# Kernel optimization log

Measured on AMD Instinct MI355X. Metric: run time of the kernel, lower is better.

Reference implementation:

```python
import jax, jax.numpy as jnp
import numpy as np

EMBED_DIM = 1024
NUM_HEADS = 16
HEAD_DIM = EMBED_DIM // NUM_HEADS  # 64


def setup_inputs() -> dict:
    key = jax.random.key(0)
    ks = jax.random.split(key, 9)
    B, S, D, Hd = 2, 2048, EMBED_DIM, HEAD_DIM
    s_in = 1.0 / np.sqrt(D)
    s_out = 1.0 / np.sqrt(D)
    return {
        "x": jax.random.normal(ks[0], (B, S, D), dtype=jnp.float32),
        # weights stored [in, out] (transpose of torch Linear.weight)
        "wq": jax.random.uniform(ks[1], (D, D), jnp.float32, -s_in, s_in),
        "bq": jax.random.uniform(ks[2], (D,), jnp.float32, -s_in, s_in),
        "wk": jax.random.uniform(ks[3], (D, Hd), jnp.float32, -s_in, s_in),
        "bk": jax.random.uniform(ks[4], (Hd,), jnp.float32, -s_in, s_in),
        "wv": jax.random.uniform(ks[5], (D, Hd), jnp.float32, -s_in, s_in),
        "bv": jax.random.uniform(ks[6], (Hd,), jnp.float32, -s_in, s_in),
        "wo": jax.random.uniform(ks[7], (D, D), jnp.float32, -s_out, s_out),
        "bo": jax.random.uniform(ks[8], (D,), jnp.float32, -s_out, s_out),
    }


def reference(x, wq, bq, wk, bk, wv, bv, wo, bo):
    B, S, D = x.shape
    H, Hd = NUM_HEADS, HEAD_DIM
    q = (x @ wq + bq).reshape(B, S, H, Hd)  # per-head queries
    k = x @ wk + bk                          # shared single-head keys  [B,S,Hd]
    v = x @ wv + bv                          # shared single-head values [B,S,Hd]
    # NOTE: original scales by embed_dim**-0.5 (not head_dim) — keep faithful.
    scores = jnp.einsum('bqhd,bkd->bhqk', q, k) / jnp.sqrt(jnp.float32(D))
    attn = jax.nn.softmax(scores, axis=-1)
    out = jnp.einsum('bhqk,bkd->bqhd', attn, v).reshape(B, S, D)
    return out @ wo + bo
```

## Files before the change

### kernel.cpp

```cpp
#include <hip/hip_runtime.h>

typedef unsigned short ushort_t;
typedef __attribute__((ext_vector_type(8))) short short8;
typedef __attribute__((ext_vector_type(4))) float f32x4;

#define EMBED 1024
#define NHEADS 16
#define HDIM 64
#define SEQ 2048
#define BATCH 2
#define BS (BATCH*SEQ)
#define QSCALE 0.045084234f

static __device__ __forceinline__ ushort_t f2b(float x) {
    union { float f; unsigned u; } v; v.f = x;
    unsigned r = v.u + 0x7FFFu + ((v.u >> 16) & 1u);
    return (ushort_t)(r >> 16);
}

static __device__ __forceinline__ void gload_lds16(const void* g, void* l) {
    __builtin_amdgcn_global_load_lds(
        (const __attribute__((address_space(1))) void*)g,
        (__attribute__((address_space(3))) void*)l, 16, 0, 0);
}

static __device__ __forceinline__ float exp2_raw(float x) {
    float r;
    asm("v_exp_f32 %0, %1" : "=v"(r) : "v"(x));
    return r;
}

__global__ __launch_bounds__(256) void prep_kernel(
    const float* __restrict__ x,
    const float* __restrict__ wq, const float* __restrict__ wk,
    const float* __restrict__ wv, const float* __restrict__ wo,
    ushort_t* __restrict__ xb, ushort_t* __restrict__ wqkv_t,
    ushort_t* __restrict__ wo_t)
{
    __shared__ float LsT[64][65];
    const int bid = blockIdx.x;
    const int t = threadIdx.x;

    if (bid < 2048) {
        const size_t i = ((size_t)bid * 256 + t) * 8;
        float4 f0 = *reinterpret_cast<const float4*>(x + i);
        float4 f1 = *reinterpret_cast<const float4*>(x + i + 4);
        short8 h;
        h[0] = (short)f2b(f0.x); h[1] = (short)f2b(f0.y);
        h[2] = (short)f2b(f0.z); h[3] = (short)f2b(f0.w);
        h[4] = (short)f2b(f1.x); h[5] = (short)f2b(f1.y);
        h[6] = (short)f2b(f1.z); h[7] = (short)f2b(f1.w);
        *reinterpret_cast<short8*>(xb + i) = h;
        return;
    }

    const float* src; ushort_t* dst; int N, bx, by;
    if (bid < 2304)      { int r = bid - 2048; src = wq; dst = wqkv_t;            N = 1024; bx = r & 15; by = r >> 4; }
    else if (bid < 2320) { int r = bid - 2304; src = wk; dst = wqkv_t + 1024*1024; N = 64;  bx = 0;      by = r; }
    else if (bid < 2336) { int r = bid - 2320; src = wv; dst = wqkv_t + 1088*1024; N = 64;  bx = 0;      by = r; }
    else                 { int r = bid - 2336; src = wo; dst = wo_t;              N = 1024; bx = r & 15; by = r >> 4; }
    const int n0 = bx * 64, k0 = by * 64;
    const int rr0 = t >> 4;
    const int c4 = (t & 15) * 4;
    #pragma unroll
    for (int rr = 0; rr < 4; ++rr) {
        float4 f = *reinterpret_cast<const float4*>(
            src + (size_t)(k0 + rr0 + rr * 16) * N + n0 + c4);
        LsT[c4 + 0][rr0 + rr * 16] = f.x;
        LsT[c4 + 1][rr0 + rr * 16] = f.y;
        LsT[c4 + 2][rr0 + rr * 16] = f.z;
        LsT[c4 + 3][rr0 + rr * 16] = f.w;
    }
    __syncthreads();
    const int rn = t >> 2;
    const int c16 = (t & 3) * 16;
    ushort_t* d = dst + (size_t)(n0 + rn) * 1024 + k0 + c16;
    short8 h0, h1;
    #pragma unroll
    for (int i = 0; i < 8; ++i) h0[i] = (short)f2b(LsT[rn][c16 + i]);
    #pragma unroll
    for (int i = 0; i < 8; ++i) h1[i] = (short)f2b(LsT[rn][c16 + 8 + i]);
    *reinterpret_cast<short8*>(d) = h0;
    *reinterpret_cast<short8*>(d + 8) = h1;
}

template<int MODE>
__global__ __launch_bounds__(256, 3) void mfma_gemm(
    const ushort_t* __restrict__ A, const ushort_t* __restrict__ Bt,
    const float* __restrict__ b0, const float* __restrict__ b1,
    const float* __restrict__ b2,
    float* __restrict__ Of, ushort_t* __restrict__ Oq,
    ushort_t* __restrict__ Okb, ushort_t* __restrict__ Ovt)
{
    __shared__ char smem[49152];

    const int tid = threadIdx.x;
    const int lane = tid & 63;
    const int w = tid >> 6;
    const int g = lane >> 4;
    const int c = lane & 15;
    const int rowBase = blockIdx.y * 128;
    const int colBase = blockIdx.x * 64;

    const int lr = lane >> 3;
    const int so = ((lane & 7) * 16) ^ (lr << 4);

    const char* Abase = (const char*)A + (size_t)rowBase * 2048;
    const char* Bbase = (const char*)Bt + (size_t)colBase * 2048;

    f32x4 acc[2][4];
    #pragma unroll
    for (int i = 0; i < 2; ++i)
        #pragma unroll
        for (int j = 0; j < 4; ++j)
            acc[i][j] = (f32x4){0.f, 0.f, 0.f, 0.f};

    #define STAGE(step, buf) do {                                              \
        char* T_ = smem + (buf) * 24576;                                       \
        const size_t kb_ = (size_t)(step) * 128;                               \
        _Pragma("unroll")                                                      \
        for (int u = 0; u < 4; ++u) {                                          \
            const int ca = 4 * w + u;                                          \
            gload_lds16(Abase + (size_t)(ca * 8 + lr) * 2048 + kb_ + so,       \
                        T_ + ca * 1024);                                       \
        }                                                                      \
        _Pragma("unroll")                                                      \
        for (int u = 0; u < 2; ++u) {                                          \
            const int cb = 2 * w + u;                                          \
            gload_lds16(Bbase + (size_t)(cb * 8 + lr) * 2048 + kb_ + so,       \
                        T_ + 16384 + cb * 1024);                               \
        }                                                                      \
    } while (0)

    STAGE(0, 0);
    __syncthreads();

    for (int i = 0; i < 16; ++i) {
        const int cur = i & 1;
        if (i < 15) STAGE(i + 1, cur ^ 1);

        const char* As = smem + cur * 24576;
        const char* Bs = As + 16384;
        #pragma unroll
        for (int ks = 0; ks < 2; ++ks) {
            short8 af[2], bf[4];
            #pragma unroll
            for (int mt = 0; mt < 2; ++mt) {
                const int row = w * 32 + mt * 16 + c;
                af[mt] = *reinterpret_cast<const short8*>(
                    As + row * 128 + ((ks * 64 + g * 16) ^ ((row & 7) << 4)));
            }
            #pragma unroll
            for (int nt = 0; nt < 4; ++nt) {
                const int row = nt * 16 + c;
                bf[nt] = *reinterpret_cast<const short8*>(
                    Bs + row * 128 + ((ks * 64 + g * 16) ^ ((row & 7) << 4)));
            }
            #pragma unroll
            for (int mt = 0; mt < 2; ++mt)
                #pragma unroll
                for (int nt = 0; nt < 4; ++nt)
                    acc[mt][nt] = __builtin_amdgcn_mfma_f32_16x16x32_bf16(
                        af[mt], bf[nt], acc[mt][nt], 0, 0, 0);
        }

        __syncthreads();
    }
    #undef STAGE

    #pragma unroll
    for (int nt = 0; nt < 4; ++nt) {
        const int colAbs = colBase + nt * 16 + c;
        #pragma unroll
        for (int mt = 0; mt < 2; ++mt) {
            const int rowA = rowBase + w * 32 + mt * 16 + g * 4;
            #pragma unroll
            for (int r = 0; r < 4; ++r) {
                const float v = acc[mt][nt][r];
                const int row = rowA + r;
                if (MODE == 2) {
                    Of[(size_t)row * 1024 + colAbs] = v + b0[colAbs];
                } else {
                    if (colAbs < 1024) {
                        Oq[(size_t)row * 1024 + colAbs] = f2b((v + b0[colAbs]) * QSCALE);
                    } else if (colAbs < 1088) {
                        const int kc = colAbs - 1024;
                        Okb[(size_t)row * 64 + kc] = f2b(v + b1[kc]);
                    } else {
                        const int hd = colAbs - 1088;
                        const int bb = row >> 11, s = row & 2047;
                        Ovt[((((size_t)bb * 32 + (s >> 6)) * 4 + (hd >> 4)) * 16
                             + (hd & 15)) * 64 + (s & 63)] = f2b(v + b2[hd]);
                    }
                }
            }
        }
    }
}

#define PSWZ(row, kbyte) ((row) * 128 + ((kbyte) ^ (((row) & 7) << 4)))

__global__ __launch_bounds__(512, 4) void attn_mfma_kernel(
    const ushort_t* __restrict__ q,
    const ushort_t* __restrict__ kb,
    const ushort_t* __restrict__ vt,
    ushort_t* __restrict__ aout)
{
    __shared__ char smem[81920];
    char* Ks0 = smem;
    char* Ks1 = smem + 16384;
    char* Vs0 = smem + 32768;
    char* Vs1 = smem + 49152;

    const int tid = threadIdx.x;
    const int lane = tid & 63;
    const int w = tid >> 6;
    const int g = lane >> 4;
    const int c = lane & 15;
    const int bid = blockIdx.x;
    const int qt = bid & 31;
    const int hp = (bid >> 5) & 7;
    const int b = bid >> 8;
    const int q0 = qt * 64;
    const int h = hp * 2 + (w >> 2);
    const int wq = w & 3;

    char* pl = smem + 65536 + (w << 11);

    short8 bq[2];
    {
        const size_t qrow = (size_t)(b * SEQ + q0 + wq * 16 + c) * 1024 + h * 64;
        bq[0] = *reinterpret_cast<const short8*>(q + qrow + g * 8);
        bq[1] = *reinterpret_cast<const short8*>(q + qrow + 32 + g * 8);
    }

    short8 vone;
    #pragma unroll
    for (int i = 0; i < 8; ++i) vone[i] = (short)0x3F80;

    const char* kbb = (const char*)kb + (size_t)b * SEQ * 128;
    const char* vbb = (const char*)vt + (size_t)b * 262144;

    const int lr = lane >> 3;
    const int so = ((lane & 7) * 16) ^ (lr << 4);

    f32x4 oacc[4];
    #pragma unroll
    for (int i = 0; i < 4; ++i) oacc[i] = (f32x4){0.f, 0.f, 0.f, 0.f};
    f32x4 lacc = (f32x4){0.f, 0.f, 0.f, 0.f};

    #pragma unroll
    for (int u = 0; u < 4; ++u) {
        const int ch = w * 4 + u;
        const int cc = ch & 15;
        const size_t srcoff = (size_t)(cc * 8 + lr) * 128 + so;
        if (ch < 16) gload_lds16(kbb + srcoff, Ks0 + cc * 1024);
        else         gload_lds16(vbb + srcoff, Vs0 + cc * 1024);
    }
    __syncthreads();

    const int csw = (c & 7) << 4;

    for (int kt = 0; kt < SEQ / 128; ++kt) {
        char* ksb = (kt & 1) ? Ks1 : Ks0;
        char* vsb = (kt & 1) ? Vs1 : Vs0;
        char* ksn = (kt & 1) ? Ks0 : Ks1;
        char* vsn = (kt & 1) ? Vs0 : Vs1;

        {
            const int ktn = (kt < SEQ / 128 - 1) ? kt + 1 : kt;
            const char* gKt = kbb + (size_t)ktn * 16384;
            const char* gVt = vbb + (size_t)ktn * 16384;
            #pragma unroll
            for (int u = 0; u < 4; ++u) {
                const int ch = w * 4 + u;
                const int cc = ch & 15;
                const size_t srcoff = (size_t)(cc * 8 + lr) * 128 + so;
                if (ch < 16) gload_lds16(gKt + srcoff, ksn + cc * 1024);
                else         gload_lds16(gVt + srcoff, vsn + cc * 1024);
            }
        }

        #pragma unroll
        for (int sub = 0; sub < 2; ++sub) {
            const char* ksub = ksb + sub * 8192;
            const char* vsub = vsb + sub * 8192;

            f32x4 sacc[4];
            __builtin_amdgcn_s_setprio(1);
            #pragma unroll
            for (int mt = 0; mt < 4; ++mt) {
                const char* kr = ksub + (mt * 16 + c) * 128;
                short8 k0 = *reinterpret_cast<const short8*>(kr + ((g * 16) ^ csw));
                short8 k1 = *reinterpret_cast<const short8*>(kr + ((64 + g * 16) ^ csw));
                f32x4 z = (f32x4){0.f, 0.f, 0.f, 0.f};
                z = __builtin_amdgcn_mfma_f32_16x16x32_bf16(k0, bq[0], z, 0, 0, 0);
                z = __builtin_amdgcn_mfma_f32_16x16x32_bf16(k1, bq[1], z, 0, 0, 0);
                sacc[mt] = z;
            }
            __builtin_amdgcn_s_setprio(0);

            #pragma unroll
            for (int mt = 0; mt < 4; ++mt) {
                const float p0 = exp2_raw(sacc[mt][0]);
                const float p1 = exp2_raw(sacc[mt][1]);
                const float p2 = exp2_raw(sacc[mt][2]);
                const float p3 = exp2_raw(sacc[mt][3]);
                uint2 pk;
                asm("v_cvt_pk_bf16_f32 %0, %1, %2" : "=v"(pk.x) : "v"(p0), "v"(p1));
                asm("v_cvt_pk_bf16_f32 %0, %1, %2" : "=v"(pk.y) : "v"(p2), "v"(p3));
                *reinterpret_cast<uint2*>(pl + PSWZ(c, mt * 32 + g * 8)) = pk;
            }

            #pragma unroll
            for (int ks = 0; ks < 2; ++ks) {
                short8 pf = *reinterpret_cast<const short8*>(pl + PSWZ(c, ks * 64 + g * 16));
                __builtin_amdgcn_s_setprio(1);
                #pragma unroll
                for (int mt = 0; mt < 4; ++mt) {
                    short8 vf = *reinterpret_cast<const short8*>(
                        vsub + (mt * 16 + c) * 128 + ((ks * 64 + g * 16) ^ csw));
                    oacc[mt] = __builtin_amdgcn_mfma_f32_16x16x32_bf16(vf, pf, oacc[mt], 0, 0, 0);
                }
                lacc = __builtin_amdgcn_mfma_f32_16x16x32_bf16(vone, pf, lacc, 0, 0, 0);
                __builtin_amdgcn_s_setprio(0);
            }
        }

        __syncthreads();
    }

    const float linv = 1.0f / lacc[0];
    #pragma unroll
    for (int mt = 0; mt < 4; ++mt) {
        uint2 ok;
        ok.x = (unsigned)f2b(oacc[mt][0] * linv) | ((unsigned)f2b(oacc[mt][1] * linv) << 16);
        ok.y = (unsigned)f2b(oacc[mt][2] * linv) | ((unsigned)f2b(oacc[mt][3] * linv) << 16);
        *reinterpret_cast<uint2*>(pl + PSWZ(c, mt * 32 + g * 8)) = ok;
    }
    {
        const int qr = lane >> 2, ch = lane & 3;
        uint4 d0 = *reinterpret_cast<const uint4*>(pl + PSWZ(qr, ch * 32));
        uint4 d1 = *reinterpret_cast<const uint4*>(pl + PSWZ(qr, ch * 32 + 16));
        ushort_t* dst = aout + (size_t)(b * SEQ + q0 + wq * 16 + qr) * 1024 + h * 64 + ch * 16;
        *reinterpret_cast<uint4*>(dst) = d0;
        *reinterpret_cast<uint4*>(dst + 8) = d1;
    }
}

extern "C" void kernel_launch(void* const* d_in, const int* in_sizes, int n_in,
                              void* d_out, int out_size, void* d_ws, size_t ws_size,
                              hipStream_t stream) {
    const float* x  = (const float*)d_in[0];
    const float* wq = (const float*)d_in[1];
    const float* bq = (const float*)d_in[2];
    const float* wk = (const float*)d_in[3];
    const float* bk = (const float*)d_in[4];
    const float* wv = (const float*)d_in[5];
    const float* bv = (const float*)d_in[6];
    const float* wo = (const float*)d_in[7];
    const float* bo = (const float*)d_in[8];
    float* out = (float*)d_out;

    ushort_t* ws     = (ushort_t*)d_ws;
    ushort_t* wqkv_t = ws;
    ushort_t* wo_t   = wqkv_t + 1152 * 1024;
    ushort_t* kbuf   = wo_t + 1024 * 1024;
    ushort_t* vtb    = kbuf + (size_t)BS * 64;
    ushort_t* qabuf  = vtb + (size_t)BS * 64;
    ushort_t* xb     = (ushort_t*)d_out;

    prep_kernel<<<2592, 256, 0, stream>>>(x, wq, wk, wv, wo, xb, wqkv_t, wo_t);

    mfma_gemm<0><<<dim3(18, 32), 256, 0, stream>>>(xb, wqkv_t, bq, bk, bv,
                                                   nullptr, qabuf, kbuf, vtb);
    attn_mfma_kernel<<<BATCH * (NHEADS / 2) * (SEQ / 64), 512, 0, stream>>>(
        qabuf, kbuf, vtb, qabuf);
    mfma_gemm<2><<<dim3(16, 32), 256, 0, stream>>>(qabuf, wo_t, bo, nullptr, nullptr,
                                                   out, nullptr, nullptr, nullptr);
}
```

Baseline: 92.53 us.

## Process two query row groups per wave in attention to reuse K/V fragments

The attention kernel now launches 256-thread blocks where each wave handles 32 query rows (two 16-row groups) instead of 16. Each K and V fragment read from LDS feeds two MFMAs, halving LDS traffic per unit of work, and each thread issues twice as many async global-to-LDS loads. The cost is doubled accumulator and score registers per wave and half as many waves per block to hide latency. The occupancy hint drops from 4 to 2 blocks.

New measurement: 92.13 us. About the same (-0.4%).

```diff
diff --git a/kernel.cpp b/kernel.cpp
--- a/kernel.cpp
+++ b/kernel.cpp
@@ -200,7 +200,7 @@
 
 #define PSWZ(row, kbyte) ((row) * 128 + ((kbyte) ^ (((row) & 7) << 4)))
 
-__global__ __launch_bounds__(512, 4) void attn_mfma_kernel(
+__global__ __launch_bounds__(256, 2) void attn_mfma_kernel(
     const ushort_t* __restrict__ q,
     const ushort_t* __restrict__ kb,
     const ushort_t* __restrict__ vt,
@@ -222,16 +222,17 @@
     const int hp = (bid >> 5) & 7;
     const int b = bid >> 8;
     const int q0 = qt * 64;
-    const int h = hp * 2 + (w >> 2);
-    const int wq = w & 3;
-
-    char* pl = smem + 65536 + (w << 11);
-
-    short8 bq[2];
-    {
-        const size_t qrow = (size_t)(b * SEQ + q0 + wq * 16 + c) * 1024 + h * 64;
-        bq[0] = *reinterpret_cast<const short8*>(q + qrow + g * 8);
-        bq[1] = *reinterpret_cast<const short8*>(q + qrow + 32 + g * 8);
+    const int h = hp * 2 + (w >> 1);
+    const int wq = w & 1;
+
+    char* pl = smem + 65536 + (w << 12);
+
+    short8 bq[2][2];
+    #pragma unroll
+    for (int rg = 0; rg < 2; ++rg) {
+        const size_t qrow = (size_t)(b * SEQ + q0 + wq * 32 + rg * 16 + c) * 1024 + h * 64;
+        bq[rg][0] = *reinterpret_cast<const short8*>(q + qrow + g * 8);
+        bq[rg][1] = *reinterpret_cast<const short8*>(q + qrow + 32 + g * 8);
     }
 
     short8 vone;
@@ -244,14 +245,18 @@
     const int lr = lane >> 3;
     const int so = ((lane & 7) * 16) ^ (lr << 4);
 
-    f32x4 oacc[4];
-    #pragma unroll
-    for (int i = 0; i < 4; ++i) oacc[i] = (f32x4){0.f, 0.f, 0.f, 0.f};
-    f32x4 lacc = (f32x4){0.f, 0.f, 0.f, 0.f};
-
-    #pragma unroll
-    for (int u = 0; u < 4; ++u) {
-        const int ch = w * 4 + u;
+    f32x4 oacc[2][4];
+    #pragma unroll
+    for (int rg = 0; rg < 2; ++rg)
+        #pragma unroll
+        for (int i = 0; i < 4; ++i) oacc[rg][i] = (f32x4){0.f, 0.f, 0.f, 0.f};
+    f32x4 lacc[2];
+    lacc[0] = (f32x4){0.f, 0.f, 0.f, 0.f};
+    lacc[1] = (f32x4){0.f, 0.f, 0.f, 0.f};
+
+    #pragma unroll
+    for (int u = 0; u < 8; ++u) {
+        const int ch = w * 8 + u;
         const int cc = ch & 15;
         const size_t srcoff = (size_t)(cc * 8 + lr) * 128 + so;
         if (ch < 16) gload_lds16(kbb + srcoff, Ks0 + cc * 1024);
@@ -272,8 +277,8 @@
             const char* gKt = kbb + (size_t)ktn * 16384;
             const char* gVt = vbb + (size_t)ktn * 16384;
             #pragma unroll
-            for (int u = 0; u < 4; ++u) {
-                const int ch = w * 4 + u;
+            for (int u = 0; u < 8; ++u) {
+                const int ch = w * 8 + u;
                 const int cc = ch & 15;
                 const size_t srcoff = (size_t)(cc * 8 + lr) * 128 + so;
                 if (ch < 16) gload_lds16(gKt + srcoff, ksn + cc * 1024);
@@ -286,43 +291,53 @@
             const char* ksub = ksb + sub * 8192;
             const char* vsub = vsb + sub * 8192;
 
-            f32x4 sacc[4];
+            f32x4 sacc[2][4];
             __builtin_amdgcn_s_setprio(1);
             #pragma unroll
             for (int mt = 0; mt < 4; ++mt) {
                 const char* kr = ksub + (mt * 16 + c) * 128;
                 short8 k0 = *reinterpret_cast<const short8*>(kr + ((g * 16) ^ csw));
                 short8 k1 = *reinterpret_cast<const short8*>(kr + ((64 + g * 16) ^ csw));
-                f32x4 z = (f32x4){0.f, 0.f, 0.f, 0.f};
-                z = __builtin_amdgcn_mfma_f32_16x16x32_bf16(k0, bq[0], z, 0, 0, 0);
-                z = __builtin_amdgcn_mfma_f32_16x16x32_bf16(k1, bq[1], z, 0, 0, 0);
-                sacc[mt] = z;
+                #pragma unroll
+                for (int rg = 0; rg < 2; ++rg) {
+                    f32x4 z = (f32x4){0.f, 0.f, 0.f, 0.f};
+                    z = __builtin_amdgcn_mfma_f32_16x16x32_bf16(k0, bq[rg][0], z, 0, 0, 0);
+                    z = __builtin_amdgcn_mfma_f32_16x16x32_bf16(k1, bq[rg][1], z, 0, 0, 0);
+                    sacc[rg][mt] = z;
+                }
             }
             __builtin_amdgcn_s_setprio(0);
 
             #pragma unroll
-            for (int mt = 0; mt < 4; ++mt) {
-                const float p0 = exp2_raw(sacc[mt][0]);
-                const float p1 = exp2_raw(sacc[mt][1]);
-                const float p2 = exp2_raw(sacc[mt][2]);
-                const float p3 = exp2_raw(sacc[mt][3]);
-                uint2 pk;
-                asm("v_cvt_pk_bf16_f32 %0, %1, %2" : "=v"(pk.x) : "v"(p0), "v"(p1));
-                asm("v_cvt_pk_bf16_f32 %0, %1, %2" : "=v"(pk.y) : "v"(p2), "v"(p3));
-                *reinterpret_cast<uint2*>(pl + PSWZ(c, mt * 32 + g * 8)) = pk;
+            for (int rg = 0; rg < 2; ++rg) {
+                char* prg = pl + rg * 2048;
+                #pragma unroll
+                for (int mt = 0; mt < 4; ++mt) {
+                    const float p0 = exp2_raw(sacc[rg][mt][0]);
+                    const float p1 = exp2_raw(sacc[rg][mt][1]);
+                    const float p2 = exp2_raw(sacc[rg][mt][2]);
+                    const float p3 = exp2_raw(sacc[rg][mt][3]);
+                    uint2 pk;
+                    asm("v_cvt_pk_bf16_f32 %0, %1, %2" : "=v"(pk.x) : "v"(p0), "v"(p1));
+                    asm("v_cvt_pk_bf16_f32 %0, %1, %2" : "=v"(pk.y) : "v"(p2), "v"(p3));
+                    *reinterpret_cast<uint2*>(prg + PSWZ(c, mt * 32 + g * 8)) = pk;
+                }
             }
 
             #pragma unroll
             for (int ks = 0; ks < 2; ++ks) {
-                short8 pf = *reinterpret_cast<const short8*>(pl + PSWZ(c, ks * 64 + g * 16));
+                short8 pf0 = *reinterpret_cast<const short8*>(pl + PSWZ(c, ks * 64 + g * 16));
+                short8 pf1 = *reinterpret_cast<const short8*>(pl + 2048 + PSWZ(c, ks * 64 + g * 16));
                 __builtin_amdgcn_s_setprio(1);
                 #pragma unroll
                 for (int mt = 0; mt < 4; ++mt) {
                     short8 vf = *reinterpret_cast<const short8*>(
                         vsub + (mt * 16 + c) * 128 + ((ks * 64 + g * 16) ^ csw));
-                    oacc[mt] = __builtin_amdgcn_mfma_f32_16x16x32_bf16(vf, pf, oacc[mt], 0, 0, 0);
+                    oacc[0][mt] = __builtin_amdgcn_mfma_f32_16x16x32_bf16(vf, pf0, oacc[0][mt], 0, 0, 0);
+                    oacc[1][mt] = __builtin_amdgcn_mfma_f32_16x16x32_bf16(vf, pf1, oacc[1][mt], 0, 0, 0);
                 }
-                lacc = __builtin_amdgcn_mfma_f32_16x16x32_bf16(vone, pf, lacc, 0, 0, 0);
+                lacc[0] = __builtin_amdgcn_mfma_f32_16x16x32_bf16(vone, pf0, lacc[0], 0, 0, 0);
+                lacc[1] = __builtin_amdgcn_mfma_f32_16x16x32_bf16(vone, pf1, lacc[1], 0, 0, 0);
                 __builtin_amdgcn_s_setprio(0);
             }
         }
@@ -330,19 +345,22 @@
         __syncthreads();
     }
 
-    const float linv = 1.0f / lacc[0];
-    #pragma unroll
-    for (int mt = 0; mt < 4; ++mt) {
-        uint2 ok;
-        ok.x = (unsigned)f2b(oacc[mt][0] * linv) | ((unsigned)f2b(oacc[mt][1] * linv) << 16);
-        ok.y = (unsigned)f2b(oacc[mt][2] * linv) | ((unsigned)f2b(oacc[mt][3] * linv) << 16);
-        *reinterpret_cast<uint2*>(pl + PSWZ(c, mt * 32 + g * 8)) = ok;
-    }
-    {
+    #pragma unroll
+    for (int rg = 0; rg < 2; ++rg) {
+        char* prg = pl + rg * 2048;
+        const float linv = 1.0f / lacc[rg][0];
+        #pragma unroll
+        for (int mt = 0; mt < 4; ++mt) {
+            uint2 ok;
+            ok.x = (unsigned)f2b(oacc[rg][mt][0] * linv) | ((unsigned)f2b(oacc[rg][mt][1] * linv) << 16);
+            ok.y = (unsigned)f2b(oacc[rg][mt][2] * linv) | ((unsigned)f2b(oacc[rg][mt][3] * linv) << 16);
+            *reinterpret_cast<uint2*>(prg + PSWZ(c, mt * 32 + g * 8)) = ok;
+        }
         const int qr = lane >> 2, ch = lane & 3;
-        uint4 d0 = *reinterpret_cast<const uint4*>(pl + PSWZ(qr, ch * 32));
-        uint4 d1 = *reinterpret_cast<const uint4*>(pl + PSWZ(qr, ch * 32 + 16));
-        ushort_t* dst = aout + (size_t)(b * SEQ + q0 + wq * 16 + qr) * 1024 + h * 64 + ch * 16;
+        uint4 d0 = *reinterpret_cast<const uint4*>(prg + PSWZ(qr, ch * 32));
+        uint4 d1 = *reinterpret_cast<const uint4*>(prg + PSWZ(qr, ch * 32 + 16));
+        ushort_t* dst = aout + (size_t)(b * SEQ + q0 + wq * 32 + rg * 16 + qr) * 1024
+                        + h * 64 + ch * 16;
         *reinterpret_cast<uint4*>(dst) = d0;
         *reinterpret_cast<uint4*>(dst + 8) = d1;
     }
@@ -374,7 +392,7 @@
 
     mfma_gemm<0><<<dim3(18, 32), 256, 0, stream>>>(xb, wqkv_t, bq, bk, bv,
                                                    nullptr, qabuf, kbuf, vtb);
-    attn_mfma_kernel<<<BATCH * (NHEADS / 2) * (SEQ / 64), 512, 0, stream>>>(
+    attn_mfma_kernel<<<BATCH * (NHEADS / 2) * (SEQ / 64), 256, 0, stream>>>(
         qabuf, kbuf, vtb, qabuf);
     mfma_gemm<2><<<dim3(16, 32), 256, 0, stream>>>(qabuf, wo_t, bo, nullptr, nullptr,
                                                    out, nullptr, nullptr, nullptr);
```

## Keep softmax probabilities in registers by permuting V layout, drop P LDS round-trip

Applied to the files above, without the earlier changes.

The projection epilogue now writes the transposed V tile with its key index permuted within each 64-key block. This lets the exp'd score fragments from the QK MFMA be packed straight into the A operand of the PV MFMA, with no write to and read from LDS. The output accumulator is transposed so that rows are queries, and the row-sum uses per-row reciprocals. The P scratch region is removed, cutting shared memory from 80KB to 64KB, which may allow more resident blocks. The epilogue reuses the K buffer as scratch, and correctness depends on the permutation exactly matching the MFMA fragment layout.

Result: faster. 88.08 us (-4.8%).

```diff
diff --git a/kernel.cpp b/kernel.cpp
--- a/kernel.cpp
+++ b/kernel.cpp
@@ -189,8 +189,10 @@
                     } else {
                         const int hd = colAbs - 1088;
                         const int bb = row >> 11, s = row & 2047;
+                        const int key = s & 63;
+                        const int pos = (key & 0x23) | ((key & 0x0C) << 1) | ((key & 0x10) >> 2);
                         Ovt[((((size_t)bb * 32 + (s >> 6)) * 4 + (hd >> 4)) * 16
-                             + (hd & 15)) * 64 + (s & 63)] = f2b(v + b2[hd]);
+                             + (hd & 15)) * 64 + pos] = f2b(v + b2[hd]);
                     }
                 }
             }
@@ -206,7 +208,7 @@
     const ushort_t* __restrict__ vt,
     ushort_t* __restrict__ aout)
 {
-    __shared__ char smem[81920];
+    __shared__ char smem[65536];
     char* Ks0 = smem;
     char* Ks1 = smem + 16384;
     char* Vs0 = smem + 32768;
@@ -225,8 +227,6 @@
     const int h = hp * 2 + (w >> 2);
     const int wq = w & 3;
 
-    char* pl = smem + 65536 + (w << 11);
-
     short8 bq[2];
     {
         const size_t qrow = (size_t)(b * SEQ + q0 + wq * 16 + c) * 1024 + h * 64;
@@ -300,29 +300,39 @@
             }
             __builtin_amdgcn_s_setprio(0);
 
-            #pragma unroll
-            for (int mt = 0; mt < 4; ++mt) {
-                const float p0 = exp2_raw(sacc[mt][0]);
-                const float p1 = exp2_raw(sacc[mt][1]);
-                const float p2 = exp2_raw(sacc[mt][2]);
-                const float p3 = exp2_raw(sacc[mt][3]);
-                uint2 pk;
-                asm("v_cvt_pk_bf16_f32 %0, %1, %2" : "=v"(pk.x) : "v"(p0), "v"(p1));
-                asm("v_cvt_pk_bf16_f32 %0, %1, %2" : "=v"(pk.y) : "v"(p2), "v"(p3));
-                *reinterpret_cast<uint2*>(pl + PSWZ(c, mt * 32 + g * 8)) = pk;
-            }
-
+            float pe[4][4];
+            #pragma unroll
+            for (int mt = 0; mt < 4; ++mt)
+                #pragma unroll
+                for (int r = 0; r < 4; ++r)
+                    pe[mt][r] = exp2_raw(sacc[mt][r]);
+
+            union U { unsigned u[4]; short8 s8; };
+            U pa[2];
             #pragma unroll
             for (int ks = 0; ks < 2; ++ks) {
-                short8 pf = *reinterpret_cast<const short8*>(pl + PSWZ(c, ks * 64 + g * 16));
+                asm("v_cvt_pk_bf16_f32 %0, %1, %2" : "=v"(pa[ks].u[0])
+                    : "v"(pe[2*ks][0]), "v"(pe[2*ks][1]));
+                asm("v_cvt_pk_bf16_f32 %0, %1, %2" : "=v"(pa[ks].u[1])
+                    : "v"(pe[2*ks][2]), "v"(pe[2*ks][3]));
+                asm("v_cvt_pk_bf16_f32 %0, %1, %2" : "=v"(pa[ks].u[2])
+                    : "v"(pe[2*ks+1][0]), "v"(pe[2*ks+1][1]));
+                asm("v_cvt_pk_bf16_f32 %0, %1, %2" : "=v"(pa[ks].u[3])
+                    : "v"(pe[2*ks+1][2]), "v"(pe[2*ks+1][3]));
+            }
+
+            #pragma unroll
+            for (int ks = 0; ks < 2; ++ks) {
                 __builtin_amdgcn_s_setprio(1);
                 #pragma unroll
-                for (int mt = 0; mt < 4; ++mt) {
+                for (int nt = 0; nt < 4; ++nt) {
                     short8 vf = *reinterpret_cast<const short8*>(
-                        vsub + (mt * 16 + c) * 128 + ((ks * 64 + g * 16) ^ csw));
-                    oacc[mt] = __builtin_amdgcn_mfma_f32_16x16x32_bf16(vf, pf, oacc[mt], 0, 0, 0);
+                        vsub + (nt * 16 + c) * 128 + ((ks * 64 + g * 16) ^ csw));
+                    oacc[nt] = __builtin_amdgcn_mfma_f32_16x16x32_bf16(
+                        pa[ks].s8, vf, oacc[nt], 0, 0, 0);
                 }
-                lacc = __builtin_amdgcn_mfma_f32_16x16x32_bf16(vone, pf, lacc, 0, 0, 0);
+                lacc = __builtin_amdgcn_mfma_f32_16x16x32_bf16(
+                    pa[ks].s8, vone, lacc, 0, 0, 0);
                 __builtin_amdgcn_s_setprio(0);
             }
         }
@@ -330,18 +340,20 @@
         __syncthreads();
     }
 
-    const float linv = 1.0f / lacc[0];
-    #pragma unroll
-    for (int mt = 0; mt < 4; ++mt) {
-        uint2 ok;
-        ok.x = (unsigned)f2b(oacc[mt][0] * linv) | ((unsigned)f2b(oacc[mt][1] * linv) << 16);
-        ok.y = (unsigned)f2b(oacc[mt][2] * linv) | ((unsigned)f2b(oacc[mt][3] * linv) << 16);
-        *reinterpret_cast<uint2*>(pl + PSWZ(c, mt * 32 + g * 8)) = ok;
-    }
+    float linv[4];
+    #pragma unroll
+    for (int r = 0; r < 4; ++r) linv[r] = 1.0f / lacc[r];
+    char* escr = smem + (w << 11);
+    #pragma unroll
+    for (int nt = 0; nt < 4; ++nt)
+        #pragma unroll
+        for (int r = 0; r < 4; ++r)
+            *reinterpret_cast<ushort_t*>(escr + PSWZ(g * 4 + r, (nt * 16 + c) * 2)) =
+                f2b(oacc[nt][r] * linv[r]);
     {
         const int qr = lane >> 2, ch = lane & 3;
-        uint4 d0 = *reinterpret_cast<const uint4*>(pl + PSWZ(qr, ch * 32));
-        uint4 d1 = *reinterpret_cast<const uint4*>(pl + PSWZ(qr, ch * 32 + 16));
+        uint4 d0 = *reinterpret_cast<const uint4*>(escr + PSWZ(qr, ch * 32));
+        uint4 d1 = *reinterpret_cast<const uint4*>(escr + PSWZ(qr, ch * 32 + 16));
         ushort_t* dst = aout + (size_t)(b * SEQ + q0 + wq * 16 + qr) * 1024 + h * 64 + ch * 16;
         *reinterpret_cast<uint4*>(dst) = d0;
         *reinterpret_cast<uint4*>(dst + 8) = d1;
```
